# Kernel optimization log

Hardware: AMD Instinct MI355X
Metric: run time of the kernel (lower is better)

## Reference

```python
import jax, jax.numpy as jnp
import numpy as np

B, C, H, W = 8, 512, 32, 32
NUM_HEADS = 8


def setup_inputs() -> dict:
    key = jax.random.key(0)
    ks = jax.random.split(key, 7)
    s = 0.02
    return {
        "x": jax.random.normal(ks[0], (B, C, H, W), dtype=jnp.float32),
        "Wq": jax.random.normal(ks[1], (C, C), dtype=jnp.float32) * s,
        "bq": jax.random.normal(ks[2], (C,), dtype=jnp.float32) * s,
        "Wk": jax.random.normal(ks[3], (C, C), dtype=jnp.float32) * s,
        "bk": jax.random.normal(ks[4], (C,), dtype=jnp.float32) * s,
        "Wv": jax.random.normal(ks[5], (C, C), dtype=jnp.float32) * s,
        "bv": jax.random.normal(ks[6], (C,), dtype=jnp.float32) * s,
        "gamma": jnp.zeros((1,), dtype=jnp.float32),
    }


def reference(x, Wq, bq, Wk, bk, Wv, bv, gamma):
    b, c, h, w = x.shape
    nh = NUM_HEADS
    hd = c // nh
    n = h * w

    def proj(Wt, bt):
        # 1x1 conv == per-pixel linear: [b,c,h,w] x [o,c] -> [b,o,h,w]
        return jnp.einsum('bchw,oc->bohw', x, Wt) + bt[None, :, None, None]

    q = proj(Wq, bq).reshape(b, nh, hd, n).transpose(0, 1, 3, 2)  # [b,nh,n,hd]
    k = proj(Wk, bk).reshape(b, nh, hd, n)                         # [b,nh,hd,n]
    v = proj(Wv, bv).reshape(b, nh, hd, n).transpose(0, 1, 3, 2)   # [b,nh,n,hd]

    energy = jnp.einsum('bhnd,bhdm->bhnm', q, k)  # NOTE: no 1/sqrt(d) scale (faithful)
    attention = jax.nn.softmax(energy, axis=-1)
    out = jnp.einsum('bhnm,bhmd->bhnd', attention, v)  # [b,nh,n,hd]
    out = out.transpose(0, 1, 3, 2).reshape(b, c, h, w)
    return gamma * out + x
```

## Files before the change

### kernel.cpp

```cpp
#include <hip/hip_runtime.h>
#include <cstdint>
#include <cstddef>

typedef float floatx4 __attribute__((ext_vector_type(4)));
typedef short shortx4 __attribute__((ext_vector_type(4)));
typedef short shortx8 __attribute__((ext_vector_type(8)));
typedef int   intx2  __attribute__((ext_vector_type(2)));

#define LDS_AS __attribute__((address_space(3)))
#define GLB_AS __attribute__((address_space(1)))

#define MFMA_16x16x32_BF16(A, B, C) __builtin_amdgcn_mfma_f32_16x16x32_bf16(A, B, C, 0, 0, 0)

#if defined(__HIP_DEVICE_COMPILE__)
  #if __has_builtin(__builtin_amdgcn_mfma_f32_16x16x16bf16_1k)
    #define MFMA_16x16x16_BF16(A, B, C) __builtin_amdgcn_mfma_f32_16x16x16bf16_1k(A, B, C, 0, 0, 0)
  #else
    #error "gfx950 device pass lacks __builtin_amdgcn_mfma_f32_16x16x16bf16_1k"
  #endif
#else
  #define MFMA_16x16x16_BF16(A, B, C) (C)
#endif

#define LOG2E 1.44269504088896340736f

__device__ __forceinline__ unsigned short f2bf(float f) {
    unsigned int u = __float_as_uint(f);
    u += 0x7fffu + ((u >> 16) & 1u);
    return (unsigned short)(u >> 16);
}

__device__ __forceinline__ float exp2f_fast(float x) {
#if defined(__HIP_DEVICE_COMPILE__) && __has_builtin(__builtin_amdgcn_exp2f)
    return __builtin_amdgcn_exp2f(x);
#else
    return exp2f(x);
#endif
}

__device__ __forceinline__ shortx4 pk4(float a, float b, float c, float d) {
#if defined(__HIP_DEVICE_COMPILE__) && __has_builtin(__builtin_amdgcn_cvt_pk_bf16_f32)
    typedef __bf16 bf16x2_t __attribute__((ext_vector_type(2)));
    bf16x2_t lo = __builtin_amdgcn_cvt_pk_bf16_f32(a, b);
    bf16x2_t hi = __builtin_amdgcn_cvt_pk_bf16_f32(c, d);
    intx2 p; p[0] = __builtin_bit_cast(int, lo); p[1] = __builtin_bit_cast(int, hi);
    return __builtin_bit_cast(shortx4, p);
#else
    unsigned int ua = __float_as_uint(a), ub = __float_as_uint(b);
    unsigned int uc = __float_as_uint(c), ud = __float_as_uint(d);
    intx2 p;
    p[0] = (int)((ua >> 16) | (ub & 0xffff0000u));
    p[1] = (int)((uc >> 16) | (ud & 0xffff0000u));
    return __builtin_bit_cast(shortx4, p);
#endif
}

__device__ __forceinline__ void gll16(const void* g, void* l) {
    __builtin_amdgcn_global_load_lds((const GLB_AS uint32_t*)g, (LDS_AS uint32_t*)l, 16, 0, 0);
}


__global__ __launch_bounds__(256) void prep_kernel(
    const float* __restrict__ x,
    const float* __restrict__ Wq, const float* __restrict__ Wk, const float* __restrict__ Wv,
    unsigned short* __restrict__ xT, unsigned short* __restrict__ Wb)
{
    const int bid = blockIdx.x;
    const int t = threadIdx.x;
    if (bid < 1024) {
        __shared__ alignas(16) unsigned short sT[64][72];
        const int b = bid >> 7, rem = bid & 127;
        const int c0 = (rem >> 4) * 64, p0 = (rem & 15) * 64;
        const int cl = (t >> 4) * 4, p4 = (t & 15) * 4;
        float4 v[4];
#pragma unroll
        for (int di = 0; di < 4; ++di)
            v[di] = *(const float4*)(x + (size_t)(b * 512 + c0 + cl + di) * 1024 + p0 + p4);
#pragma unroll
        for (int j = 0; j < 4; ++j) {
            shortx4 pk;
#pragma unroll
            for (int dd = 0; dd < 4; ++dd)
                pk[dd] = (short)f2bf(((const float*)&v[dd])[j]);
            *(shortx4*)&sT[p4 + j][cl] = pk;
        }
        __syncthreads();
        const int p = t >> 2, ch = (t & 3) * 16;
        const size_t base = ((size_t)b * 1024 + p0 + p) * 512 + c0 + ch;
        *(shortx8*)&xT[base] = *(const shortx8*)&sT[p][ch];
        *(shortx8*)&xT[base + 8] = *(const shortx8*)&sT[p][ch + 8];
    } else {
        const int wb = bid - 1024;
        const int mat = wb >> 6;
        const float* src = (mat == 0) ? Wq : (mat == 1) ? Wk : Wv;
        const int off0 = (wb & 63) * 4096;
#pragma unroll
        for (int r = 0; r < 4; ++r) {
            const int idx = off0 + r * 1024 + t * 4;
            const float4 v = *(const float4*)(src + idx);
            shortx4 pk;
            pk[0] = (short)f2bf(v.x); pk[1] = (short)f2bf(v.y);
            pk[2] = (short)f2bf(v.z); pk[3] = (short)f2bf(v.w);
            *(shortx4*)&Wb[(size_t)mat * 262144 + idx] = pk;
        }
    }
}

__global__ __launch_bounds__(256, 4) void proj_kernel(
    const unsigned short* __restrict__ Wb, const unsigned short* __restrict__ xT,
    const float* __restrict__ bq, const float* __restrict__ bk, const float* __restrict__ bv,
    unsigned short* __restrict__ Qg, unsigned short* __restrict__ Kg,
    unsigned short* __restrict__ Vg)
{
    __shared__ union {
        struct { unsigned short W[2][3][32][32]; unsigned short X[2][128][32]; } s;
        unsigned short Ep[128][40];
    } u;

    const int tid = threadIdx.x;
    const int w = tid >> 6, lane = tid & 63;
    const int quad = lane >> 4, l16 = lane & 15;
    const int id = blockIdx.x;
    const int oo = id & 1;
    const int p0 = ((id >> 1) & 7) * 128;
    const int bh = id >> 4, b = bh >> 3, h = bh & 7;
    const int o0 = h * 64 + oo * 32;

    floatx4 acc[3][2][2];
#pragma unroll
    for (int t = 0; t < 3; ++t) {
        const float* bsrc = (t == 0) ? bq : (t == 1) ? bk : bv;
#pragma unroll
        for (int ot = 0; ot < 2; ++ot) {
            floatx4 bi;
#pragma unroll
            for (int i = 0; i < 4; ++i)
                bi[i] = bsrc[o0 + ot * 16 + quad * 4 + i];
#pragma unroll
            for (int pt = 0; pt < 2; ++pt) acc[t][ot][pt] = bi;
        }
    }

    auto stage = [&](int ks, int bfi) {
        const int c0 = ks * 32;
#pragma unroll
        for (int jj = 0; jj < 4; ++jj) {
            const int j = jj * 4 + w;
            if (j < 6) {
                const int rf0 = j * 16;
                const int rf = rf0 + (lane >> 2);
                const int mt = rf >> 5, r = rf & 31;
                const int cl = (lane & 3) ^ (r & 3);
                gll16(Wb + (size_t)mt * 262144 + (size_t)(o0 + r) * 512 + c0 + cl * 8,
                      &u.s.W[bfi][0][0][0] + rf0 * 32);
            } else if (j < 14) {
                const int r0 = (j - 6) * 16;
                const int r = r0 + (lane >> 2);
                const int cl = (lane & 3) ^ (r & 3);
                gll16(xT + (size_t)(b * 1024 + p0 + r) * 512 + c0 + cl * 8,
                      &u.s.X[bfi][0][0] + r0 * 32);
            }
        }
    };

    stage(0, 0);
    for (int ks = 0; ks < 16; ++ks) {
        __syncthreads();
        if (ks + 1 < 16) stage(ks + 1, (ks + 1) & 1);
        const int bfi = ks & 1;
        shortx8 af[3][2], bx[2];
#pragma unroll
        for (int t = 0; t < 3; ++t)
#pragma unroll
            for (int ot = 0; ot < 2; ++ot) {
                const int r = ot * 16 + l16;
                const int pc = quad ^ (r & 3);
                af[t][ot] = *(const shortx8*)&u.s.W[bfi][t][r][pc * 8];
            }
#pragma unroll
        for (int pt = 0; pt < 2; ++pt) {
            const int r = w * 32 + pt * 16 + l16;
            const int pc = quad ^ (r & 3);
            bx[pt] = *(const shortx8*)&u.s.X[bfi][r][pc * 8];
        }
#pragma unroll
        for (int t = 0; t < 3; ++t)
#pragma unroll
            for (int ot = 0; ot < 2; ++ot)
#pragma unroll
                for (int pt = 0; pt < 2; ++pt)
                    acc[t][ot][pt] = MFMA_16x16x32_BF16(af[t][ot], bx[pt], acc[t][ot][pt]);
    }

#pragma unroll
    for (int ot = 0; ot < 2; ++ot)
#pragma unroll
        for (int pt = 0; pt < 2; ++pt)
#pragma unroll
            for (int i = 0; i < 4; ++i) {
                const int d = oo * 32 + ot * 16 + quad * 4 + i;
                const int p = p0 + w * 32 + pt * 16 + l16;
                Vg[((size_t)bh * 64 + d) * 1024 + p] = f2bf(acc[2][ot][pt][i]);
            }
#pragma unroll
    for (int t = 0; t < 2; ++t) {
        const float scale = (t == 0) ? LOG2E : 1.0f;
        __syncthreads();
#pragma unroll
        for (int ot = 0; ot < 2; ++ot)
#pragma unroll
            for (int pt = 0; pt < 2; ++pt)
#pragma unroll
                for (int i = 0; i < 4; ++i)
                    u.Ep[w * 32 + pt * 16 + l16][ot * 16 + quad * 4 + i] =
                        f2bf(acc[t][ot][pt][i] * scale);
        __syncthreads();
        unsigned short* G = (t == 0) ? Qg : Kg;
        const int p = tid >> 1, ch = (tid & 1) * 16;
        const size_t base = ((size_t)bh * 1024 + p0 + p) * 64 + oo * 32 + ch;
        *(shortx8*)&G[base]     = *(const shortx8*)&u.Ep[p][ch];
        *(shortx8*)&G[base + 8] = *(const shortx8*)&u.Ep[p][ch + 8];
    }
}

__global__ __launch_bounds__(64, 2) void attn_kernel(
    const unsigned short* __restrict__ Qg, const unsigned short* __restrict__ Kg,
    const unsigned short* __restrict__ Vg, const float* __restrict__ x,
    const float* __restrict__ gamma, float* __restrict__ out)
{
    __shared__ alignas(16) unsigned short sK[64][64];
    __shared__ alignas(16) unsigned short sV[64][64];

    const int lane = threadIdx.x;
    const int quad = lane >> 4, l16 = lane & 15;
    const int bh = blockIdx.x, b = bh >> 3, h = bh & 7;
    const int pw = blockIdx.y * 32;

    const unsigned short* KgB = Kg + (size_t)bh * 65536;
    const unsigned short* VgB = Vg + (size_t)bh * 65536;

    shortx8 aq[2][2];
#pragma unroll
    for (int pt = 0; pt < 2; ++pt)
#pragma unroll
        for (int ks = 0; ks < 2; ++ks)
            aq[pt][ks] = *(const shortx8*)
                &Qg[((size_t)bh * 1024 + pw + pt * 16 + l16) * 64 + ks * 32 + quad * 8];

    floatx4 oacc[2][4];
#pragma unroll
    for (int pt = 0; pt < 2; ++pt)
#pragma unroll
        for (int dt = 0; dt < 4; ++dt) oacc[pt][dt] = (floatx4)0.0f;
    floatx4 lacc[2] = {(floatx4)0.0f, (floatx4)0.0f};
    const shortx4 ones4 = {(short)0x3F80, (short)0x3F80, (short)0x3F80, (short)0x3F80};

    const int rstage = lane >> 3;
    const int clx    = lane & 7;

    for (int kt = 0; kt < 16; ++kt) {
        const int m0 = kt * 64;
        asm volatile("s_waitcnt lgkmcnt(0)" ::: "memory");
#pragma unroll
        for (int ii = 0; ii < 8; ++ii) {
            const int r = ii * 8 + rstage;
            const int cl = clx ^ (r & 7);
            gll16(KgB + (size_t)(m0 + r) * 64 + cl * 8, &sK[0][0] + ii * 512);
        }
#pragma unroll
        for (int ii = 0; ii < 8; ++ii) {
            const int r = ii * 8 + rstage;
            const int cl = clx ^ (r & 7);
            gll16(VgB + (size_t)r * 1024 + m0 + cl * 8, &sV[0][0] + ii * 512);
        }
        asm volatile("s_waitcnt vmcnt(8)" ::: "memory");

        floatx4 s[2][4];
#pragma unroll
        for (int pt = 0; pt < 2; ++pt)
#pragma unroll
            for (int nt = 0; nt < 4; ++nt) s[pt][nt] = (floatx4)0.0f;
#pragma unroll
        for (int nt = 0; nt < 4; ++nt)
#pragma unroll
            for (int ks = 0; ks < 2; ++ks) {
                const int r = nt * 16 + l16;
                const int pc = (ks * 4 + quad) ^ (r & 7);
                const shortx8 ak = *(const shortx8*)&sK[r][pc * 8];
#pragma unroll
                for (int pt = 0; pt < 2; ++pt)
                    s[pt][nt] = MFMA_16x16x32_BF16(ak, aq[pt][ks], s[pt][nt]);
            }

        shortx4 bp[2][4];
#pragma unroll
        for (int pt = 0; pt < 2; ++pt)
#pragma unroll
            for (int mt = 0; mt < 4; ++mt) {
                float e0 = exp2f_fast(s[pt][mt][0]);
                float e1 = exp2f_fast(s[pt][mt][1]);
                float e2 = exp2f_fast(s[pt][mt][2]);
                float e3 = exp2f_fast(s[pt][mt][3]);
                bp[pt][mt] = pk4(e0, e1, e2, e3);
            }

        asm volatile("s_waitcnt vmcnt(0)" ::: "memory");

#pragma unroll
        for (int dt = 0; dt < 4; ++dt)
#pragma unroll
            for (int mt = 0; mt < 4; ++mt) {
                const int r = dt * 16 + l16;
                const int pc = (mt * 2 + (quad >> 1)) ^ (r & 7);
                const shortx4 av = *(const shortx4*)&sV[r][pc * 8 + (quad & 1) * 4];
#pragma unroll
                for (int pt = 0; pt < 2; ++pt)
                    oacc[pt][dt] = MFMA_16x16x16_BF16(av, bp[pt][mt], oacc[pt][dt]);
            }
#pragma unroll
        for (int mt = 0; mt < 4; ++mt)
#pragma unroll
            for (int pt = 0; pt < 2; ++pt)
                lacc[pt] = MFMA_16x16x16_BF16(ones4, bp[pt][mt], lacc[pt]);
    }

    const float g = gamma[0];
    const float invl[2] = {1.0f / lacc[0][0], 1.0f / lacc[1][0]};
#pragma unroll
    for (int pt = 0; pt < 2; ++pt)
#pragma unroll
        for (int dt = 0; dt < 4; ++dt)
#pragma unroll
            for (int i = 0; i < 4; ++i) {
                const int d = dt * 16 + quad * 4 + i;
                const int p = pw + pt * 16 + l16;
                const size_t idx = ((size_t)b * 512 + h * 64 + d) * 1024 + p;
                out[idx] = g * (oacc[pt][dt][i] * invl[pt]) + x[idx];
            }
}

extern "C" void kernel_launch(void* const* d_in, const int* in_sizes, int n_in,
                              void* d_out, int out_size, void* d_ws, size_t ws_size,
                              hipStream_t stream) {
    const float* x     = (const float*)d_in[0];
    const float* Wq    = (const float*)d_in[1];
    const float* bq    = (const float*)d_in[2];
    const float* Wk    = (const float*)d_in[3];
    const float* bk    = (const float*)d_in[4];
    const float* Wv    = (const float*)d_in[5];
    const float* bv    = (const float*)d_in[6];
    const float* gamma = (const float*)d_in[7];
    float* out = (float*)d_out;

    unsigned short* xT = (unsigned short*)d_ws;
    unsigned short* Wb = xT + 4194304;
    unsigned short* Qg = Wb + 786432;
    unsigned short* Kg = Qg + 4194304;
    unsigned short* Vg = Kg + 4194304;

    prep_kernel<<<1216, 256, 0, stream>>>(x, Wq, Wk, Wv, xT, Wb);
    proj_kernel<<<1024, 256, 0, stream>>>(Wb, xT, bq, bk, bv, Qg, Kg, Vg);
    attn_kernel<<<dim3(64, 32), 64, 0, stream>>>(Qg, Kg, Vg, x, gamma, out);
}
```

Baseline: 132.1 us.

## Split attention KV range across four waves and merge partials in LDS

The attention kernel moves from one 64-thread wave handling 32 queries over all 1024 keys to a 256-thread block handling 64 queries. Each of the four waves processes a quarter of the keys, and the partial outputs and row sums are reduced through a shared-memory union. The final epilogue then writes coalesced float4 stores to the output and reads x the same way. This is meant to raise per-wave K/V reuse, since each wave now serves 4 query tiles, and to shorten each wave's serial loop. The cost is more registers, a larger LDS footprint, and an extra merge phase with two block barriers.

```diff
diff --git a/kernel.cpp b/kernel.cpp
--- a/kernel.cpp
+++ b/kernel.cpp
@@ -223,85 +223,91 @@
     }
 }
 
-__global__ __launch_bounds__(64, 2) void attn_kernel(
+__global__ __launch_bounds__(256, 2) void attn_kernel(
     const unsigned short* __restrict__ Qg, const unsigned short* __restrict__ Kg,
     const unsigned short* __restrict__ Vg, const float* __restrict__ x,
     const float* __restrict__ gamma, float* __restrict__ out)
 {
-    __shared__ alignas(16) unsigned short sK[64][64];
-    __shared__ alignas(16) unsigned short sV[64][64];
-
-    const int lane = threadIdx.x;
+    __shared__ union {
+        unsigned short KV[4][8192];
+        struct { float O[4][64][68]; float L[4][64]; } mg;
+    } u;
+
+    const int tid = threadIdx.x;
+    const int w = tid >> 6, lane = tid & 63;
     const int quad = lane >> 4, l16 = lane & 15;
     const int bh = blockIdx.x, b = bh >> 3, h = bh & 7;
-    const int pw = blockIdx.y * 32;
+    const int p0 = blockIdx.y * 64;
 
     const unsigned short* KgB = Kg + (size_t)bh * 65536;
     const unsigned short* VgB = Vg + (size_t)bh * 65536;
 
-    shortx8 aq[2][2];
-#pragma unroll
-    for (int pt = 0; pt < 2; ++pt)
+    shortx8 aq[4][2];
+#pragma unroll
+    for (int qt = 0; qt < 4; ++qt)
 #pragma unroll
         for (int ks = 0; ks < 2; ++ks)
-            aq[pt][ks] = *(const shortx8*)
-                &Qg[((size_t)bh * 1024 + pw + pt * 16 + l16) * 64 + ks * 32 + quad * 8];
-
-    floatx4 oacc[2][4];
-#pragma unroll
-    for (int pt = 0; pt < 2; ++pt)
-#pragma unroll
-        for (int dt = 0; dt < 4; ++dt) oacc[pt][dt] = (floatx4)0.0f;
-    floatx4 lacc[2] = {(floatx4)0.0f, (floatx4)0.0f};
+            aq[qt][ks] = *(const shortx8*)
+                &Qg[((size_t)bh * 1024 + p0 + qt * 16 + l16) * 64 + ks * 32 + quad * 8];
+
+    floatx4 oacc[4][4];
+#pragma unroll
+    for (int qt = 0; qt < 4; ++qt)
+#pragma unroll
+        for (int dt = 0; dt < 4; ++dt) oacc[qt][dt] = (floatx4)0.0f;
+    floatx4 lacc[4];
+#pragma unroll
+    for (int qt = 0; qt < 4; ++qt) lacc[qt] = (floatx4)0.0f;
     const shortx4 ones4 = {(short)0x3F80, (short)0x3F80, (short)0x3F80, (short)0x3F80};
 
-    const int rstage = lane >> 3;
-    const int clx    = lane & 7;
-
-    for (int kt = 0; kt < 16; ++kt) {
-        const int m0 = kt * 64;
+    unsigned short* Kb = &u.KV[w][0];
+    unsigned short* Vb = &u.KV[w][4096];
+    const int rstage = lane >> 3, clx = lane & 7;
+
+    for (int it = 0; it < 4; ++it) {
+        const int m0 = (w * 4 + it) * 64;
         asm volatile("s_waitcnt lgkmcnt(0)" ::: "memory");
 #pragma unroll
         for (int ii = 0; ii < 8; ++ii) {
             const int r = ii * 8 + rstage;
             const int cl = clx ^ (r & 7);
-            gll16(KgB + (size_t)(m0 + r) * 64 + cl * 8, &sK[0][0] + ii * 512);
+            gll16(KgB + (size_t)(m0 + r) * 64 + cl * 8, Kb + ii * 512);
         }
 #pragma unroll
         for (int ii = 0; ii < 8; ++ii) {
             const int r = ii * 8 + rstage;
             const int cl = clx ^ (r & 7);
-            gll16(VgB + (size_t)r * 1024 + m0 + cl * 8, &sV[0][0] + ii * 512);
+            gll16(VgB + (size_t)r * 1024 + m0 + cl * 8, Vb + ii * 512);
         }
         asm volatile("s_waitcnt vmcnt(8)" ::: "memory");
 
-        floatx4 s[2][4];
-#pragma unroll
-        for (int pt = 0; pt < 2; ++pt)
-#pragma unroll
-            for (int nt = 0; nt < 4; ++nt) s[pt][nt] = (floatx4)0.0f;
+        floatx4 s[4][4];
+#pragma unroll
+        for (int qt = 0; qt < 4; ++qt)
+#pragma unroll
+            for (int nt = 0; nt < 4; ++nt) s[qt][nt] = (floatx4)0.0f;
 #pragma unroll
         for (int nt = 0; nt < 4; ++nt)
 #pragma unroll
             for (int ks = 0; ks < 2; ++ks) {
                 const int r = nt * 16 + l16;
                 const int pc = (ks * 4 + quad) ^ (r & 7);
-                const shortx8 ak = *(const shortx8*)&sK[r][pc * 8];
-#pragma unroll
-                for (int pt = 0; pt < 2; ++pt)
-                    s[pt][nt] = MFMA_16x16x32_BF16(ak, aq[pt][ks], s[pt][nt]);
-            }
-
-        shortx4 bp[2][4];
-#pragma unroll
-        for (int pt = 0; pt < 2; ++pt)
+                const shortx8 ak = *(const shortx8*)&Kb[r * 64 + pc * 8];
+#pragma unroll
+                for (int qt = 0; qt < 4; ++qt)
+                    s[qt][nt] = MFMA_16x16x32_BF16(ak, aq[qt][ks], s[qt][nt]);
+            }
+
+        shortx4 bp[4][4];
+#pragma unroll
+        for (int qt = 0; qt < 4; ++qt)
 #pragma unroll
             for (int mt = 0; mt < 4; ++mt) {
-                float e0 = exp2f_fast(s[pt][mt][0]);
-                float e1 = exp2f_fast(s[pt][mt][1]);
-                float e2 = exp2f_fast(s[pt][mt][2]);
-                float e3 = exp2f_fast(s[pt][mt][3]);
-                bp[pt][mt] = pk4(e0, e1, e2, e3);
+                float e0 = exp2f_fast(s[qt][mt][0]);
+                float e1 = exp2f_fast(s[qt][mt][1]);
+                float e2 = exp2f_fast(s[qt][mt][2]);
+                float e3 = exp2f_fast(s[qt][mt][3]);
+                bp[qt][mt] = pk4(e0, e1, e2, e3);
             }
 
         asm volatile("s_waitcnt vmcnt(0)" ::: "memory");
@@ -312,31 +318,54 @@
             for (int mt = 0; mt < 4; ++mt) {
                 const int r = dt * 16 + l16;
                 const int pc = (mt * 2 + (quad >> 1)) ^ (r & 7);
-                const shortx4 av = *(const shortx4*)&sV[r][pc * 8 + (quad & 1) * 4];
-#pragma unroll
-                for (int pt = 0; pt < 2; ++pt)
-                    oacc[pt][dt] = MFMA_16x16x16_BF16(av, bp[pt][mt], oacc[pt][dt]);
+                const shortx4 av = *(const shortx4*)&Vb[r * 64 + pc * 8 + (quad & 1) * 4];
+#pragma unroll
+                for (int qt = 0; qt < 4; ++qt)
+                    oacc[qt][dt] = MFMA_16x16x16_BF16(av, bp[qt][mt], oacc[qt][dt]);
             }
 #pragma unroll
         for (int mt = 0; mt < 4; ++mt)
 #pragma unroll
-            for (int pt = 0; pt < 2; ++pt)
-                lacc[pt] = MFMA_16x16x16_BF16(ones4, bp[pt][mt], lacc[pt]);
-    }
+            for (int qt = 0; qt < 4; ++qt)
+                lacc[qt] = MFMA_16x16x16_BF16(ones4, bp[qt][mt], lacc[qt]);
+    }
+
+    __syncthreads();
+#pragma unroll
+    for (int qt = 0; qt < 4; ++qt)
+#pragma unroll
+        for (int dt = 0; dt < 4; ++dt)
+            *(floatx4*)&u.mg.O[w][qt * 16 + l16][dt * 16 + quad * 4] = oacc[qt][dt];
+    if (quad == 0) {
+#pragma unroll
+        for (int qt = 0; qt < 4; ++qt)
+            u.mg.L[w][qt * 16 + l16] = lacc[qt][0];
+    }
+    __syncthreads();
 
     const float g = gamma[0];
-    const float invl[2] = {1.0f / lacc[0][0], 1.0f / lacc[1][0]};
-#pragma unroll
-    for (int pt = 0; pt < 2; ++pt)
-#pragma unroll
-        for (int dt = 0; dt < 4; ++dt)
-#pragma unroll
-            for (int i = 0; i < 4; ++i) {
-                const int d = dt * 16 + quad * 4 + i;
-                const int p = pw + pt * 16 + l16;
-                const size_t idx = ((size_t)b * 512 + h * 64 + d) * 1024 + p;
-                out[idx] = g * (oacc[pt][dt][i] * invl[pt]) + x[idx];
-            }
+    const int d = tid >> 2, pch = (tid & 3) * 16;
+#pragma unroll
+    for (int j = 0; j < 4; ++j) {
+        const int pb = pch + j * 4;
+        float o0 = 0, o1 = 0, o2 = 0, o3 = 0;
+        float l0 = 0, l1 = 0, l2 = 0, l3 = 0;
+#pragma unroll
+        for (int ww = 0; ww < 4; ++ww) {
+            o0 += u.mg.O[ww][pb + 0][d]; o1 += u.mg.O[ww][pb + 1][d];
+            o2 += u.mg.O[ww][pb + 2][d]; o3 += u.mg.O[ww][pb + 3][d];
+            l0 += u.mg.L[ww][pb + 0];    l1 += u.mg.L[ww][pb + 1];
+            l2 += u.mg.L[ww][pb + 2];    l3 += u.mg.L[ww][pb + 3];
+        }
+        const size_t idx = ((size_t)(b * 512 + h * 64 + d)) * 1024 + p0 + pb;
+        const float4 xv = *(const float4*)(x + idx);
+        float4 yv;
+        yv.x = g * (o0 / l0) + xv.x;
+        yv.y = g * (o1 / l1) + xv.y;
+        yv.z = g * (o2 / l2) + xv.z;
+        yv.w = g * (o3 / l3) + xv.w;
+        *(float4*)(out + idx) = yv;
+    }
 }
 
 extern "C" void kernel_launch(void* const* d_in, const int* in_sizes, int n_in,
@@ -360,5 +389,5 @@
 
     prep_kernel<<<1216, 256, 0, stream>>>(x, Wq, Wk, Wv, xT, Wb);
     proj_kernel<<<1024, 256, 0, stream>>>(Wb, xT, bq, bk, bv, Qg, Kg, Vg);
-    attn_kernel<<<dim3(64, 32), 64, 0, stream>>>(Qg, Kg, Vg, x, gamma, out);
-}
+    attn_kernel<<<dim3(64, 16), 256, 0, stream>>>(Qg, Kg, Vg, x, gamma, out);
+}
```

Result: slower. 136.7 us (+3.5%).
